# Kernel tuning notes

Hardware: AMD Instinct MI355X
Metric: run time of the kernel (lower is better)

Reference implementation:

```python
import jax, jax.numpy as jnp
import numpy as np

B = 8          # graphs per batch
N_PER = 8192   # nodes per graph (equal-sized graphs -> static topk shapes)
N = B * N_PER  # 65536 total nodes
DEG = 16
E = DEG * N    # 1,048,576 edges
C = 64         # conv_width


def setup_inputs() -> dict:
    key = jax.random.key(0)
    ks = jax.random.split(key, 32)
    epg = E // B
    g = jnp.arange(E, dtype=jnp.int32) // epg            # graph id per edge
    src = jax.random.randint(ks[0], (E,), 0, N_PER, dtype=jnp.int32) + g * N_PER
    dst = jax.random.randint(ks[1], (E,), 0, N_PER, dtype=jnp.int32) + g * N_PER

    def w(k, shape, fan_in):
        return (jax.random.normal(k, shape) / np.sqrt(fan_in)).astype(jnp.float32)

    inp = {
        "x": jax.random.normal(ks[2], (N, 2), dtype=jnp.float32),
        "edge_index": jnp.stack([src, dst]),
        # SAGEConv i: out = mean_agg @ wl + x @ wr + b
        "w1l": w(ks[3], (2, C), 2),  "w1r": w(ks[4], (2, C), 2),  "b1": jnp.zeros((C,), jnp.float32),
        "w2l": w(ks[5], (C, C), C),  "w2r": w(ks[6], (C, C), C),  "b2": jnp.zeros((C,), jnp.float32),
        "w3l": w(ks[7], (C, C), C),  "w3r": w(ks[8], (C, C), C),  "b3": jnp.zeros((C,), jnp.float32),
        # GCNConv
        "w4": w(ks[9], (C, C), C),   "b4": jnp.zeros((C,), jnp.float32),
        # TopKPooling score vectors
        "p1": w(ks[10], (C,), C), "p2": w(ks[11], (C,), C),
        "p3": w(ks[12], (C,), C), "p4": w(ks[13], (C,), C),
        # MLP head
        "lw1": w(ks[14], (2 * C, 128), 2 * C), "lb1": jnp.zeros((128,), jnp.float32),
        "lw2": w(ks[15], (128, 64), 128),      "lb2": jnp.zeros((64,), jnp.float32),
        "lw3": w(ks[16], (64, 1), 64),         "lb3": jnp.zeros((1,), jnp.float32),
    }
    return inp


def _sage(x, src, dst, em, wl, wr, b):
    # PyG SAGEConv: lin_l(mean of in-neighbors) + lin_r(x); masked edges contribute 0
    n = x.shape[0]
    s = jax.ops.segment_sum(x[src] * em[:, None], dst, num_segments=n)
    cnt = jax.ops.segment_sum(em, dst, num_segments=n)
    mean = s / jnp.maximum(cnt, 1.0)[:, None]
    return mean @ wl + x @ wr + b


def _gcn(x, src, dst, em, w, b):
    # PyG GCNConv with added self-loops, symmetric normalization
    n = x.shape[0]
    xw = x @ w
    deg = jax.ops.segment_sum(em, dst, num_segments=n) + 1.0  # +1 self-loop
    dinv = jax.lax.rsqrt(deg)
    coef = (dinv[src] * dinv[dst] * em)[:, None]
    agg = jax.ops.segment_sum(xw[src] * coef, dst, num_segments=n)
    return agg + xw / deg[:, None] + b  # self-loop term: deg^-0.5 * deg^-0.5


def _pool(x, src, dst, em, p, nb):
    # TopKPooling(ratio=0.5): score = x.p/||p||, keep top half per graph, scale by tanh
    n = x.shape[0]
    npg = n // nb
    k = npg // 2
    score = x @ p / jnp.linalg.norm(p)
    _, idx = jax.lax.top_k(score.reshape(nb, npg), k)          # [nb, k] local idx
    perm = (idx + (jnp.arange(nb, dtype=idx.dtype) * npg)[:, None]).reshape(-1)
    xn = x[perm] * jnp.tanh(score[perm])[:, None]
    o2n = jnp.full((n,), -1, jnp.int32).at[perm].set(jnp.arange(nb * k, dtype=jnp.int32))
    ns, nd = o2n[src], o2n[dst]
    nm = em * ((ns >= 0) & (nd >= 0)).astype(em.dtype)         # filter_adj via mask
    return xn, jnp.maximum(ns, 0), jnp.maximum(nd, 0), nm


def _readout(x, nb):
    # cat([global_max_pool, global_mean_pool])
    npg = x.shape[0] // nb
    batch = jnp.repeat(jnp.arange(nb), npg)
    mx = jax.ops.segment_max(x, batch, num_segments=nb)
    mn = jax.ops.segment_sum(x, batch, num_segments=nb) / npg
    return jnp.concatenate([mx, mn], axis=1)


def reference(x, edge_index, w1l, w1r, b1, w2l, w2r, b2, w3l, w3r, b3, w4, b4,
              p1, p2, p3, p4, lw1, lb1, lw2, lb2, lw3, lb3):
    src, dst = edge_index[0], edge_index[1]
    em = jnp.ones((src.shape[0],), jnp.float32)

    h = jax.nn.relu(_sage(x, src, dst, em, w1l, w1r, b1))
    h, src, dst, em = _pool(h, src, dst, em, p1, B)
    x1 = _readout(h, B)

    h = jax.nn.relu(_sage(h, src, dst, em, w2l, w2r, b2))
    h, src, dst, em = _pool(h, src, dst, em, p2, B)
    x2 = _readout(h, B)

    h = jax.nn.relu(_sage(h, src, dst, em, w3l, w3r, b3))
    h, src, dst, em = _pool(h, src, dst, em, p3, B)
    x3 = _readout(h, B)  # computed but unused, matching original (x = x1 + x2)

    h = jax.nn.relu(_gcn(h, src, dst, em, w4, b4))
    h, src, dst, em = _pool(h, src, dst, em, p4, B)
    x4 = _readout(h, B)  # computed but unused, matching original

    z = x1 + x2
    z = jax.nn.relu(z @ lw1 + lb1)
    z = jax.nn.relu(z @ lw2 + lb2)
    return z @ lw3 + lb3  # [B, 1]
```

## Files before the change

kernel.cpp:

```cpp
#include <hip/hip_runtime.h>
#include <stdint.h>
#include <math.h>

#define NB 8
#define NPG0 8192
#define EPG 131072
#define P1 16
#define MAXDEG 64

__global__ __launch_bounds__(1024)
void k_aggp(const int* __restrict__ src, const int* __restrict__ dst,
            const float* __restrict__ x, float* __restrict__ partial)
{
    __shared__ float acc[3 * 2048];
    int b = blockIdx.x;
    int g = b >> 6, qq = (b >> 4) & 3, sl = b & 15;
    int tid = threadIdx.x;
    float4* acc4 = (float4*)acc;
    float4 z4 = make_float4(0.f, 0.f, 0.f, 0.f);
    acc4[tid] = z4;
    if (tid < 512) acc4[1024 + tid] = z4;
    __syncthreads();
    int e0 = g * EPG + sl * (EPG / P1);
    int nbase = g * NPG0 + qq * 2048;
    const float2* x2 = reinterpret_cast<const float2*>(x);
    #pragma unroll
    for (int k = 0; k < 2; ++k) {
        int e = e0 + (k * 1024 + tid) * 4;
        int4 d4 = *reinterpret_cast<const int4*>(dst + e);
        unsigned l0 = (unsigned)(d4.x - nbase), l1 = (unsigned)(d4.y - nbase);
        unsigned l2 = (unsigned)(d4.z - nbase), l3 = (unsigned)(d4.w - nbase);
        bool v0 = l0 < 2048u, v1 = l1 < 2048u, v2 = l2 < 2048u, v3 = l3 < 2048u;
        if (v0 | v1 | v2 | v3) {
            int4 s4 = *reinterpret_cast<const int4*>(src + e);
            if (v0) { float2 xv = x2[s4.x]; atomicAdd(&acc[l0], xv.x);
                      atomicAdd(&acc[2048 + l0], xv.y); atomicAdd(&acc[4096 + l0], 1.0f); }
            if (v1) { float2 xv = x2[s4.y]; atomicAdd(&acc[l1], xv.x);
                      atomicAdd(&acc[2048 + l1], xv.y); atomicAdd(&acc[4096 + l1], 1.0f); }
            if (v2) { float2 xv = x2[s4.z]; atomicAdd(&acc[l2], xv.x);
                      atomicAdd(&acc[2048 + l2], xv.y); atomicAdd(&acc[4096 + l2], 1.0f); }
            if (v3) { float2 xv = x2[s4.w]; atomicAdd(&acc[l3], xv.x);
                      atomicAdd(&acc[2048 + l3], xv.y); atomicAdd(&acc[4096 + l3], 1.0f); }
        }
    }
    __syncthreads();
    float4* o = (float4*)(partial + (size_t)b * 6144);
    o[tid] = acc4[tid];
    if (tid < 512) o[1024 + tid] = acc4[1024 + tid];
}

__global__ __launch_bounds__(256)
void k_sage1f(const float* __restrict__ partial, const float* __restrict__ x,
              const float* __restrict__ w1l, const float* __restrict__ w1r,
              const float* __restrict__ b1, const float* __restrict__ p1,
              float2* __restrict__ mv, float* __restrict__ s1)
{
    int tid = threadIdx.x;
    int node = blockIdx.x * 256 + tid;
    int g = node >> 13, local = node & (NPG0 - 1);
    int qq = local >> 11, ll = local & 2047;
    const float* p = partial + (size_t)(g * 64 + qq * 16) * 6144 + ll;
    float s0 = 0.f, s1v = 0.f, sc = 0.f;
    #pragma unroll
    for (int q = 0; q < 16; ++q) {
        const float* pq = p + (size_t)q * 6144;
        s0 += pq[0]; s1v += pq[2048]; sc += pq[4096];
    }
    float inv = 1.0f / fmaxf(sc, 1.0f);
    float m0 = s0 * inv, m1 = s1v * inv;
    float2 xv = reinterpret_cast<const float2*>(x)[node];
    mv[node] = make_float2(m0, m1);
    float num = 0.f, nrm = 0.f;
    #pragma unroll 8
    for (int c = 0; c < 64; ++c) {
        float h = fmaxf(m0 * w1l[c] + m1 * w1l[64 + c]
                      + xv.x * w1r[c] + xv.y * w1r[64 + c] + b1[c], 0.0f);
        float pv = p1[c];
        num += h * pv; nrm += pv * pv;
    }
    s1[node] = num / sqrtf(nrm);
}

__device__ __forceinline__ unsigned scan1024(unsigned val, volatile unsigned* ws)
{
    int tid = threadIdx.x, lane = tid & 63, wid = tid >> 6;
    unsigned sc = val;
    #pragma unroll
    for (int off = 1; off < 64; off <<= 1) {
        unsigned t = __shfl_up(sc, off);
        if (lane >= off) sc += t;
    }
    if (lane == 63) ws[wid] = sc;
    __syncthreads();
    if (tid < 16) {
        unsigned w = ws[tid];
        #pragma unroll
        for (int off = 1; off < 16; off <<= 1) {
            unsigned t = __shfl_up(w, off);
            if (tid >= off) w += t;
        }
        ws[tid] = w;
    }
    __syncthreads();
    return sc + (wid ? ws[wid - 1] : 0u);
}

__global__ __launch_bounds__(1024)
void k_pool1(const float* __restrict__ score, int* __restrict__ n2o,
             int* __restrict__ o2n, int K, int* __restrict__ zbuf)
{
    const int NPG = 8192;
    __shared__ unsigned key[NPG];
    __shared__ unsigned hist[1024];
    __shared__ unsigned ws[16];
    __shared__ unsigned long long cand[1024];
    __shared__ int sT1, sR1, sT2, sR2, selCnt, c3;
    int g = blockIdx.x, tid = threadIdx.x;
    for (int i = tid; i < 4096; i += 1024) zbuf[g * 4096 + i] = 0;
    if (tid == 0) { selCnt = 0; c3 = 0; }
    hist[tid] = 0u;
    for (int i = tid; i < NPG; i += 1024) o2n[g * NPG + i] = -1;
    __syncthreads();
    for (int i = tid; i < NPG; i += 1024) {
        unsigned b = __float_as_uint(score[g * NPG + i]);
        unsigned u = (b & 0x80000000u) ? ~b : (b | 0x80000000u);
        key[i] = u;
        atomicAdd(&hist[u >> 22], 1u);
    }
    __syncthreads();
    {
        unsigned S = scan1024(hist[1023 - tid], ws);
        int b = 1023 - tid;
        unsigned h = hist[b];
        if (S >= (unsigned)K && S - h < (unsigned)K) { sT1 = b; sR1 = K - (int)(S - h); }
    }
    __syncthreads();
    int T1 = sT1, R1 = sR1;
    for (int i = tid; i < NPG; i += 1024) {
        if ((int)(key[i] >> 22) > T1) {
            int s = atomicAdd(&selCnt, 1);
            int oldid = g * NPG + i;
            n2o[g * K + s] = oldid;
            o2n[oldid] = g * K + s;
        }
    }
    __syncthreads();
    hist[tid] = 0u;
    __syncthreads();
    for (int i = tid; i < NPG; i += 1024)
        if ((int)(key[i] >> 22) == T1) atomicAdd(&hist[(key[i] >> 12) & 1023u], 1u);
    __syncthreads();
    {
        unsigned S = scan1024(hist[1023 - tid], ws);
        int b = 1023 - tid;
        unsigned h = hist[b];
        if (S >= (unsigned)R1 && S - h < (unsigned)R1) { sT2 = b; sR2 = R1 - (int)(S - h); }
    }
    __syncthreads();
    int T2 = sT2, R2 = sR2;
    for (int i = tid; i < NPG; i += 1024) {
        unsigned u = key[i];
        if ((int)(u >> 22) == T1) {
            int b2 = (int)((u >> 12) & 1023u);
            if (b2 > T2) {
                int s = atomicAdd(&selCnt, 1);
                int oldid = g * NPG + i;
                n2o[g * K + s] = oldid;
                o2n[oldid] = g * K + s;
            } else if (b2 == T2) {
                int c = atomicAdd(&c3, 1);
                if (c < 1024)
                    cand[c] = ((unsigned long long)u << 32) | (unsigned)(NPG - 1 - i);
            }
        }
    }
    __syncthreads();
    int M = min(c3, 1024);
    for (int t = tid; t < M; t += 1024) {
        unsigned long long k0 = cand[t];
        int rank = 0;
        for (int j = 0; j < M; ++j) rank += (cand[j] > k0);
        if (rank < R2) {
            int i = NPG - 1 - (int)(k0 & 0xFFFFFFFFu);
            int s = atomicAdd(&selCnt, 1);
            int oldid = g * NPG + i;
            n2o[g * K + s] = oldid;
            o2n[oldid] = g * K + s;
        }
    }
}

__global__ __launch_bounds__(1024)
void k_pool2(const float* __restrict__ score, int* __restrict__ n2o, int K)
{
    const int NPG = 4096;
    __shared__ unsigned key[NPG];
    __shared__ unsigned hist[1024];
    __shared__ unsigned ws[16];
    __shared__ unsigned long long cand[1024];
    __shared__ int sT1, sR1, sT2, sR2, selCnt, c3;
    int g = blockIdx.x, tid = threadIdx.x;
    if (tid == 0) { selCnt = 0; c3 = 0; }
    hist[tid] = 0u;
    __syncthreads();
    for (int i = tid; i < NPG; i += 1024) {
        unsigned b = __float_as_uint(score[g * NPG + i]);
        unsigned u = (b & 0x80000000u) ? ~b : (b | 0x80000000u);
        key[i] = u;
        atomicAdd(&hist[u >> 22], 1u);
    }
    __syncthreads();
    {
        unsigned S = scan1024(hist[1023 - tid], ws);
        int b = 1023 - tid;
        unsigned h = hist[b];
        if (S >= (unsigned)K && S - h < (unsigned)K) { sT1 = b; sR1 = K - (int)(S - h); }
    }
    __syncthreads();
    int T1 = sT1, R1 = sR1;
    for (int i = tid; i < NPG; i += 1024) {
        if ((int)(key[i] >> 22) > T1)
            n2o[g * K + atomicAdd(&selCnt, 1)] = g * NPG + i;
    }
    __syncthreads();
    hist[tid] = 0u;
    __syncthreads();
    for (int i = tid; i < NPG; i += 1024)
        if ((int)(key[i] >> 22) == T1) atomicAdd(&hist[(key[i] >> 12) & 1023u], 1u);
    __syncthreads();
    {
        unsigned S = scan1024(hist[1023 - tid], ws);
        int b = 1023 - tid;
        unsigned h = hist[b];
        if (S >= (unsigned)R1 && S - h < (unsigned)R1) { sT2 = b; sR2 = R1 - (int)(S - h); }
    }
    __syncthreads();
    int T2 = sT2, R2 = sR2;
    for (int i = tid; i < NPG; i += 1024) {
        unsigned u = key[i];
        if ((int)(u >> 22) == T1) {
            int b2 = (int)((u >> 12) & 1023u);
            if (b2 > T2) {
                n2o[g * K + atomicAdd(&selCnt, 1)] = g * NPG + i;
            } else if (b2 == T2) {
                int c = atomicAdd(&c3, 1);
                if (c < 1024)
                    cand[c] = ((unsigned long long)u << 32) | (unsigned)(NPG - 1 - i);
            }
        }
    }
    __syncthreads();
    int M = min(c3, 1024);
    for (int t = tid; t < M; t += 1024) {
        unsigned long long k0 = cand[t];
        int rank = 0;
        for (int j = 0; j < M; ++j) rank += (cand[j] > k0);
        if (rank < R2) {
            int i = NPG - 1 - (int)(k0 & 0xFFFFFFFFu);
            n2o[g * K + atomicAdd(&selCnt, 1)] = g * NPG + i;
        }
    }
}

__global__ __launch_bounds__(1024)
void k_mid(const float2* __restrict__ mv, const float* __restrict__ x,
           const float* __restrict__ s1, const int* __restrict__ n2o,
           const float* __restrict__ w1l, const float* __restrict__ w1r,
           const float* __restrict__ b1, int npg, float* __restrict__ hp,
           float* __restrict__ pmx, float* __restrict__ psm,
           const int* __restrict__ src, const int* __restrict__ dst,
           const int* __restrict__ o2n, int* __restrict__ cnt,
           int* __restrict__ slots)
{
    __shared__ float4 smx[1024], ssm[1024];
    int b = blockIdx.x;
    int tid = threadIdx.x;
    if (b >= 128) {
        int e = ((b - 128) * 1024 + tid) * 4;
        int4 s4 = *reinterpret_cast<const int4*>(src + e);
        int4 d4 = *reinterpret_cast<const int4*>(dst + e);
        #pragma unroll
        for (int i = 0; i < 4; ++i) {
            int sv = (i == 0) ? s4.x : (i == 1) ? s4.y : (i == 2) ? s4.z : s4.w;
            int dv = (i == 0) ? d4.x : (i == 1) ? d4.y : (i == 2) ? d4.z : d4.w;
            int ns = o2n[sv], nd = o2n[dv];
            if (ns >= 0 && nd >= 0) {
                int pos = atomicAdd(&cnt[nd], 1);
                if (pos < MAXDEG) slots[nd * MAXDEG + pos] = ns;
            }
        }
        return;
    }
    int g = b >> 4, sl = b & 15;
    int cg = tid & 15, rsl = tid >> 4;
    int rpb = npg >> 4;
    int c0 = cg * 4;
    float4 wl0 = *reinterpret_cast<const float4*>(w1l + c0);
    float4 wl1 = *reinterpret_cast<const float4*>(w1l + 64 + c0);
    float4 wr0 = *reinterpret_cast<const float4*>(w1r + c0);
    float4 wr1 = *reinterpret_cast<const float4*>(w1r + 64 + c0);
    float4 bb  = *reinterpret_cast<const float4*>(b1 + c0);
    const float2* x2 = reinterpret_cast<const float2*>(x);
    float4 mx = make_float4(-INFINITY, -INFINITY, -INFINITY, -INFINITY);
    float4 sm = make_float4(0.f, 0.f, 0.f, 0.f);
    for (int r = rsl; r < rpb; r += 64) {
        int row = g * npg + sl * rpb + r;
        int old = n2o[row];
        float2 m = mv[old];
        float2 xv = x2[old];
        float t = tanhf(s1[old]);
        float4 v;
        v.x = fmaxf(m.x * wl0.x + m.y * wl1.x + xv.x * wr0.x + xv.y * wr1.x + bb.x, 0.f) * t;
        v.y = fmaxf(m.x * wl0.y + m.y * wl1.y + xv.x * wr0.y + xv.y * wr1.y + bb.y, 0.f) * t;
        v.z = fmaxf(m.x * wl0.z + m.y * wl1.z + xv.x * wr0.z + xv.y * wr1.z + bb.z, 0.f) * t;
        v.w = fmaxf(m.x * wl0.w + m.y * wl1.w + xv.x * wr0.w + xv.y * wr1.w + bb.w, 0.f) * t;
        reinterpret_cast<float4*>(hp)[row * 16 + cg] = v;
        mx.x = fmaxf(mx.x, v.x); mx.y = fmaxf(mx.y, v.y);
        mx.z = fmaxf(mx.z, v.z); mx.w = fmaxf(mx.w, v.w);
        sm.x += v.x; sm.y += v.y; sm.z += v.z; sm.w += v.w;
    }
    smx[tid] = mx; ssm[tid] = sm;
    __syncthreads();
    for (int s = 32; s >= 1; s >>= 1) {
        if (rsl < s) {
            float4 a = smx[tid], bq = smx[tid + s * 16];
            a.x = fmaxf(a.x, bq.x); a.y = fmaxf(a.y, bq.y);
            a.z = fmaxf(a.z, bq.z); a.w = fmaxf(a.w, bq.w);
            smx[tid] = a;
            float4 c = ssm[tid], d = ssm[tid + s * 16];
            c.x += d.x; c.y += d.y; c.z += d.z; c.w += d.w;
            ssm[tid] = c;
        }
        __syncthreads();
    }
    if (rsl == 0) {
        reinterpret_cast<float4*>(pmx)[(g * 16 + sl) * 16 + cg] = smx[tid];
        reinterpret_cast<float4*>(psm)[(g * 16 + sl) * 16 + cg] = ssm[tid];
    }
}

__global__ __launch_bounds__(256)
void k_sage2(const float* __restrict__ hp, const int* __restrict__ cnt,
             const int* __restrict__ slots,
             const float* __restrict__ w2l, const float* __restrict__ w2r,
             const float* __restrict__ b2, const float* __restrict__ p2,
             float* __restrict__ h2, float* __restrict__ s2)
{
    __shared__ float Xs[64 * 128];
    __shared__ float Wt[64 * 128];
    int tid = threadIdx.x, blk = blockIdx.x;

    #pragma unroll
    for (int i = 0; i < 32; ++i) {
        int idx = i * 256 + tid;
        int k = idx >> 6, c = idx & 63;
        float w = (k < 64) ? w2l[k * 64 + c] : w2r[(k - 64) * 64 + c];
        int slot = (k >> 2) ^ ((c >> 2) & 7);
        Wt[c * 128 + slot * 4 + (k & 3)] = w;
    }

    {
        int n = tid >> 2, p = tid & 3;
        int j = blk * 64 + n;
        int dg = cnt[j];
        int lim = min(dg, MAXDEG);
        const int* sl = slots + j * MAXDEG;
        const float4* hp4 = reinterpret_cast<const float4*>(hp);
        float4 a[4];
        #pragma unroll
        for (int u = 0; u < 4; ++u) a[u] = make_float4(0.f, 0.f, 0.f, 0.f);
        int e = 0;
        for (; e + 1 < lim; e += 2) {
            int r0 = sl[e] * 16 + p * 4;
            int r1 = sl[e + 1] * 16 + p * 4;
            float4 v[4], u4[4];
            #pragma unroll
            for (int u = 0; u < 4; ++u) v[u] = hp4[r0 + u];
            #pragma unroll
            for (int u = 0; u < 4; ++u) u4[u] = hp4[r1 + u];
            #pragma unroll
            for (int u = 0; u < 4; ++u) {
                a[u].x += v[u].x + u4[u].x; a[u].y += v[u].y + u4[u].y;
                a[u].z += v[u].z + u4[u].z; a[u].w += v[u].w + u4[u].w;
            }
        }
        if (e < lim) {
            int r0 = sl[e] * 16 + p * 4;
            #pragma unroll
            for (int u = 0; u < 4; ++u) {
                float4 v = hp4[r0 + u];
                a[u].x += v.x; a[u].y += v.y; a[u].z += v.z; a[u].w += v.w;
            }
        }
        float inv = 1.0f / fmaxf((float)dg, 1.0f);
        int swz = (n >> 2) & 7;
        float4* X4 = reinterpret_cast<float4*>(Xs);
        #pragma unroll
        for (int u = 0; u < 4; ++u) {
            float4 m = a[u];
            m.x *= inv; m.y *= inv; m.z *= inv; m.w *= inv;
            X4[n * 32 + ((p * 4 + u) ^ swz)] = m;
        }
        #pragma unroll
        for (int u = 0; u < 4; ++u)
            X4[n * 32 + ((16 + p * 4 + u) ^ swz)] = hp4[j * 16 + p * 4 + u];
    }
    __syncthreads();

    int rt = tid >> 4, ct = tid & 15;
    int r0 = rt * 4, c0 = ct * 4;
    int swa = rt & 7, swb = ct & 7;
    const float4* Xf = reinterpret_cast<const float4*>(Xs);
    const float4* Wf = reinterpret_cast<const float4*>(Wt);
    float acc[4][4];
    #pragma unroll
    for (int i = 0; i < 4; ++i)
        #pragma unroll
        for (int jq = 0; jq < 4; ++jq) acc[i][jq] = 0.f;
    #pragma unroll 8
    for (int ks = 0; ks < 32; ++ks) {
        float4 aa[4], bb[4];
        #pragma unroll
        for (int i = 0; i < 4; ++i) aa[i] = Xf[(r0 + i) * 32 + (ks ^ swa)];
        #pragma unroll
        for (int jq = 0; jq < 4; ++jq) bb[jq] = Wf[(c0 + jq) * 32 + (ks ^ swb)];
        #pragma unroll
        for (int i = 0; i < 4; ++i)
            #pragma unroll
            for (int jq = 0; jq < 4; ++jq)
                acc[i][jq] += aa[i].x * bb[jq].x + aa[i].y * bb[jq].y
                            + aa[i].z * bb[jq].z + aa[i].w * bb[jq].w;
    }

    float4 b2v = reinterpret_cast<const float4*>(b2)[ct];
    float4 p2v = reinterpret_cast<const float4*>(p2)[ct];
    float nrm = p2v.x * p2v.x + p2v.y * p2v.y + p2v.z * p2v.z + p2v.w * p2v.w;
    float sp[4];
    float4* h2f = reinterpret_cast<float4*>(h2);
    #pragma unroll
    for (int i = 0; i < 4; ++i) {
        float4 o;
        o.x = fmaxf(acc[i][0] + b2v.x, 0.f);
        o.y = fmaxf(acc[i][1] + b2v.y, 0.f);
        o.z = fmaxf(acc[i][2] + b2v.z, 0.f);
        o.w = fmaxf(acc[i][3] + b2v.w, 0.f);
        h2f[(blk * 64 + r0 + i) * 16 + ct] = o;
        sp[i] = o.x * p2v.x + o.y * p2v.y + o.z * p2v.z + o.w * p2v.w;
    }
    #pragma unroll
    for (int o = 1; o < 16; o <<= 1) {
        #pragma unroll
        for (int i = 0; i < 4; ++i) sp[i] += __shfl_xor(sp[i], o);
        nrm += __shfl_xor(nrm, o);
    }
    if (ct == 0) {
        float r = rsqrtf(nrm);
        #pragma unroll
        for (int i = 0; i < 4; ++i) s2[blk * 64 + r0 + i] = sp[i] * r;
    }
}

__global__ __launch_bounds__(1024)
void k_readout_p(const float* __restrict__ h, const int* __restrict__ n2o,
                 const float* __restrict__ sc, int npg,
                 float* __restrict__ pmx, float* __restrict__ psm)
{
    int g = blockIdx.x >> 4, sl = blockIdx.x & 15;
    int tid = threadIdx.x;
    int cg = tid & 15, rsl = tid >> 4;
    int rpb = npg >> 4;
    float4 mx = make_float4(-INFINITY, -INFINITY, -INFINITY, -INFINITY);
    float4 sm = make_float4(0.f, 0.f, 0.f, 0.f);
    for (int r = rsl; r < rpb; r += 64) {
        int row = g * npg + sl * rpb + r;
        int oldid = n2o[row];
        float t = tanhf(sc[oldid]);
        float4 v = reinterpret_cast<const float4*>(h)[oldid * 16 + cg];
        v.x *= t; v.y *= t; v.z *= t; v.w *= t;
        mx.x = fmaxf(mx.x, v.x); mx.y = fmaxf(mx.y, v.y);
        mx.z = fmaxf(mx.z, v.z); mx.w = fmaxf(mx.w, v.w);
        sm.x += v.x; sm.y += v.y; sm.z += v.z; sm.w += v.w;
    }
    __shared__ float4 smx[1024], ssm[1024];
    smx[tid] = mx; ssm[tid] = sm;
    __syncthreads();
    for (int s = 32; s >= 1; s >>= 1) {
        if (rsl < s) {
            float4 a = smx[tid], b = smx[tid + s * 16];
            a.x = fmaxf(a.x, b.x); a.y = fmaxf(a.y, b.y);
            a.z = fmaxf(a.z, b.z); a.w = fmaxf(a.w, b.w);
            smx[tid] = a;
            float4 c = ssm[tid], d = ssm[tid + s * 16];
            c.x += d.x; c.y += d.y; c.z += d.z; c.w += d.w;
            ssm[tid] = c;
        }
        __syncthreads();
    }
    if (rsl == 0) {
        reinterpret_cast<float4*>(pmx)[(g * 16 + sl) * 16 + cg] = smx[tid];
        reinterpret_cast<float4*>(psm)[(g * 16 + sl) * 16 + cg] = ssm[tid];
    }
}

__global__ __launch_bounds__(128)
void k_mlp(const float* __restrict__ pmx1, const float* __restrict__ psm1,
           const float* __restrict__ pmx2, const float* __restrict__ psm2,
           int npg1, int npg2,
           const float* __restrict__ lw1, const float* __restrict__ lb1,
           const float* __restrict__ lw2, const float* __restrict__ lb2,
           const float* __restrict__ lw3, const float* __restrict__ lb3,
           float* __restrict__ out)
{
    __shared__ float z[NB][128], o1[NB][128], o2[NB][64];
    int tid = threadIdx.x;
    for (int g = 0; g < NB; ++g) {
        float v;
        if (tid < 64) {
            float m1 = -INFINITY, m2 = -INFINITY;
            #pragma unroll
            for (int sl = 0; sl < 16; ++sl) {
                m1 = fmaxf(m1, pmx1[(g * 16 + sl) * 64 + tid]);
                m2 = fmaxf(m2, pmx2[(g * 16 + sl) * 64 + tid]);
            }
            v = m1 + m2;
        } else {
            int ch = tid - 64;
            float s1 = 0.f, s2 = 0.f;
            #pragma unroll
            for (int sl = 0; sl < 16; ++sl) {
                s1 += psm1[(g * 16 + sl) * 64 + ch];
                s2 += psm2[(g * 16 + sl) * 64 + ch];
            }
            v = s1 / (float)npg1 + s2 / (float)npg2;
        }
        z[g][tid] = v;
    }
    __syncthreads();
    for (int g = 0; g < NB; ++g) {
        float a = lb1[tid];
        for (int i = 0; i < 128; ++i) a += z[g][i] * lw1[i * 128 + tid];
        o1[g][tid] = fmaxf(a, 0.0f);
    }
    __syncthreads();
    if (tid < 64) {
        for (int g = 0; g < NB; ++g) {
            float a = lb2[tid];
            for (int i = 0; i < 128; ++i) a += o1[g][i] * lw2[i * 64 + tid];
            o2[g][tid] = fmaxf(a, 0.0f);
        }
    }
    __syncthreads();
    if (tid < NB) {
        int g = tid;
        float a = lb3[0];
        for (int i = 0; i < 64; ++i) a += o2[g][i] * lw3[i];
        out[g] = a;
    }
}

extern "C" void kernel_launch(void* const* d_in, const int* in_sizes, int n_in,
                              void* d_out, int out_size, void* d_ws, size_t ws_size,
                              hipStream_t stream)
{
    (void)n_in; (void)out_size; (void)ws_size;
    const float* x   = (const float*)d_in[0];
    const int*   ei  = (const int*)d_in[1];
    const float* w1l = (const float*)d_in[2];
    const float* w1r = (const float*)d_in[3];
    const float* b1  = (const float*)d_in[4];
    const float* w2l = (const float*)d_in[5];
    const float* w2r = (const float*)d_in[6];
    const float* b2  = (const float*)d_in[7];
    const float* p1  = (const float*)d_in[13];
    const float* p2  = (const float*)d_in[14];
    const float* lw1 = (const float*)d_in[17];
    const float* lb1 = (const float*)d_in[18];
    const float* lw2 = (const float*)d_in[19];
    const float* lb2 = (const float*)d_in[20];
    const float* lw3 = (const float*)d_in[21];
    const float* lb3 = (const float*)d_in[22];

    const int N0   = in_sizes[0] / 2;
    const int E    = in_sizes[1] / 2;
    const int K1   = NPG0 / 2;
    const int N1   = NB * K1;
    const int K2   = K1 / 2;

    const int* src = ei;
    const int* dst = ei + E;

    char* w = (char*)d_ws;
    auto alloc = [&](size_t bytes) -> char* {
        char* p = w;
        w += (bytes + 255) & ~(size_t)255;
        return p;
    };
    float*  partial = (float*)alloc((size_t)NB * 4 * P1 * 6144 * 4);
    float2* mv    = (float2*)alloc((size_t)N0 * 8);
    int*    cnt2  = (int*)alloc((size_t)N1 * 4);
    int*    slots = (int*)alloc((size_t)N1 * MAXDEG * 4);
    float*  s1    = (float*)alloc((size_t)N0 * 4);
    int*    o2n1  = (int*)alloc((size_t)N0 * 4);
    int*    n2o1  = (int*)alloc((size_t)N1 * 4);
    float*  h1p   = (float*)alloc((size_t)N1 * 64 * 4);
    float*  h2    = (float*)alloc((size_t)N1 * 64 * 4);
    float*  s2    = (float*)alloc((size_t)N1 * 4);
    int*    n2o2  = (int*)alloc((size_t)(NB * K2) * 4);
    float*  pmx1  = (float*)alloc((size_t)NB * 16 * 64 * 4);
    float*  psm1  = (float*)alloc((size_t)NB * 16 * 64 * 4);
    float*  pmx2  = (float*)alloc((size_t)NB * 16 * 64 * 4);
    float*  psm2  = (float*)alloc((size_t)NB * 16 * 64 * 4);

    k_aggp<<<NB * 4 * P1, 1024, 0, stream>>>(src, dst, x, partial);
    k_sage1f<<<N0 / 256, 256, 0, stream>>>(partial, x, w1l, w1r, b1, p1, mv, s1);
    k_pool1<<<NB, 1024, 0, stream>>>(s1, n2o1, o2n1, K1, cnt2);
    k_mid<<<128 + 256, 1024, 0, stream>>>(mv, x, s1, n2o1, w1l, w1r, b1, K1,
                                          h1p, pmx1, psm1,
                                          src, dst, o2n1, cnt2, slots);
    k_sage2<<<N1 / 64, 256, 0, stream>>>(h1p, cnt2, slots, w2l, w2r, b2, p2, h2, s2);
    k_pool2<<<NB, 1024, 0, stream>>>(s2, n2o2, K2);
    k_readout_p<<<NB * 16, 1024, 0, stream>>>(h2, n2o2, s2, K2, pmx2, psm2);
    k_mlp<<<1, 128, 0, stream>>>(pmx1, psm1, pmx2, psm2, K1, K2,
                                 lw1, lb1, lw2, lb2, lw3, lb3, (float*)d_out);
}
```

Baseline: 121.9 us.

## Fuse pool2, readout and MLP into one kernel with flag-based sync

The last three launches (top-k pool of layer 2, partial readout, MLP head) become a single kernel. The first 8 blocks do per-graph selection and publish a release flag. Readout blocks spin on their graph's flag, and the last block to finish, found through an atomic counter, runs the MLP. This removes two kernel launch gaps at the tail. It relies on the producer blocks being scheduled before or alongside the spinning consumers, which risks deadlock if they are not resident together.

```diff
diff --git a/kernel.cpp b/kernel.cpp
--- a/kernel.cpp
+++ b/kernel.cpp
@@ -107,7 +107,8 @@
 
 __global__ __launch_bounds__(1024)
 void k_pool1(const float* __restrict__ score, int* __restrict__ n2o,
-             int* __restrict__ o2n, int K, int* __restrict__ zbuf)
+             int* __restrict__ o2n, int K, int* __restrict__ zbuf,
+             int* __restrict__ flags, int* __restrict__ counter)
 {
     const int NPG = 8192;
     __shared__ unsigned key[NPG];
@@ -117,6 +118,8 @@
     __shared__ int sT1, sR1, sT2, sR2, selCnt, c3;
     int g = blockIdx.x, tid = threadIdx.x;
     for (int i = tid; i < 4096; i += 1024) zbuf[g * 4096 + i] = 0;
+    if (g == 0 && tid < 8) flags[tid] = 0;
+    if (g == 0 && tid == 8) *counter = 0;
     if (tid == 0) { selCnt = 0; c3 = 0; }
     hist[tid] = 0u;
     for (int i = tid; i < NPG; i += 1024) o2n[g * NPG + i] = -1;
@@ -186,78 +189,6 @@
             int oldid = g * NPG + i;
             n2o[g * K + s] = oldid;
             o2n[oldid] = g * K + s;
-        }
-    }
-}
-
-__global__ __launch_bounds__(1024)
-void k_pool2(const float* __restrict__ score, int* __restrict__ n2o, int K)
-{
-    const int NPG = 4096;
-    __shared__ unsigned key[NPG];
-    __shared__ unsigned hist[1024];
-    __shared__ unsigned ws[16];
-    __shared__ unsigned long long cand[1024];
-    __shared__ int sT1, sR1, sT2, sR2, selCnt, c3;
-    int g = blockIdx.x, tid = threadIdx.x;
-    if (tid == 0) { selCnt = 0; c3 = 0; }
-    hist[tid] = 0u;
-    __syncthreads();
-    for (int i = tid; i < NPG; i += 1024) {
-        unsigned b = __float_as_uint(score[g * NPG + i]);
-        unsigned u = (b & 0x80000000u) ? ~b : (b | 0x80000000u);
-        key[i] = u;
-        atomicAdd(&hist[u >> 22], 1u);
-    }
-    __syncthreads();
-    {
-        unsigned S = scan1024(hist[1023 - tid], ws);
-        int b = 1023 - tid;
-        unsigned h = hist[b];
-        if (S >= (unsigned)K && S - h < (unsigned)K) { sT1 = b; sR1 = K - (int)(S - h); }
-    }
-    __syncthreads();
-    int T1 = sT1, R1 = sR1;
-    for (int i = tid; i < NPG; i += 1024) {
-        if ((int)(key[i] >> 22) > T1)
-            n2o[g * K + atomicAdd(&selCnt, 1)] = g * NPG + i;
-    }
-    __syncthreads();
-    hist[tid] = 0u;
-    __syncthreads();
-    for (int i = tid; i < NPG; i += 1024)
-        if ((int)(key[i] >> 22) == T1) atomicAdd(&hist[(key[i] >> 12) & 1023u], 1u);
-    __syncthreads();
-    {
-        unsigned S = scan1024(hist[1023 - tid], ws);
-        int b = 1023 - tid;
-        unsigned h = hist[b];
-        if (S >= (unsigned)R1 && S - h < (unsigned)R1) { sT2 = b; sR2 = R1 - (int)(S - h); }
-    }
-    __syncthreads();
-    int T2 = sT2, R2 = sR2;
-    for (int i = tid; i < NPG; i += 1024) {
-        unsigned u = key[i];
-        if ((int)(u >> 22) == T1) {
-            int b2 = (int)((u >> 12) & 1023u);
-            if (b2 > T2) {
-                n2o[g * K + atomicAdd(&selCnt, 1)] = g * NPG + i;
-            } else if (b2 == T2) {
-                int c = atomicAdd(&c3, 1);
-                if (c < 1024)
-                    cand[c] = ((unsigned long long)u << 32) | (unsigned)(NPG - 1 - i);
-            }
-        }
-    }
-    __syncthreads();
-    int M = min(c3, 1024);
-    for (int t = tid; t < M; t += 1024) {
-        unsigned long long k0 = cand[t];
-        int rank = 0;
-        for (int j = 0; j < M; ++j) rank += (cand[j] > k0);
-        if (rank < R2) {
-            int i = NPG - 1 - (int)(k0 & 0xFFFFFFFFu);
-            n2o[g * K + atomicAdd(&selCnt, 1)] = g * NPG + i;
         }
     }
 }
@@ -461,34 +392,121 @@
 }
 
 __global__ __launch_bounds__(1024)
-void k_readout_p(const float* __restrict__ h, const int* __restrict__ n2o,
-                 const float* __restrict__ sc, int npg,
-                 float* __restrict__ pmx, float* __restrict__ psm)
-{
-    int g = blockIdx.x >> 4, sl = blockIdx.x & 15;
-    int tid = threadIdx.x;
+void k_tail(const float* __restrict__ s2, const float* __restrict__ h2,
+            int* __restrict__ n2o2, int* __restrict__ flags, int* __restrict__ counter,
+            const float* __restrict__ pmx1, const float* __restrict__ psm1,
+            float* __restrict__ pmx2, float* __restrict__ psm2,
+            const float* __restrict__ lw1, const float* __restrict__ lb1,
+            const float* __restrict__ lw2, const float* __restrict__ lb2,
+            const float* __restrict__ lw3, const float* __restrict__ lb3,
+            float* __restrict__ out)
+{
+    const int NPG = 4096, K = 2048;
+    __shared__ __align__(16) char smem[33 * 1024];
+    __shared__ unsigned wsS[16];
+    __shared__ int sT1, sR1, sT2, sR2, selCnt, c3, isLast;
+    int b = blockIdx.x, tid = threadIdx.x;
+
+    if (b < 8) {
+        unsigned* key  = (unsigned*)smem;
+        unsigned* hist = (unsigned*)(smem + 16 * 1024);
+        unsigned long long* cand = (unsigned long long*)(smem + 20 * 1024);
+        int g = b;
+        if (tid == 0) { selCnt = 0; c3 = 0; }
+        hist[tid] = 0u;
+        __syncthreads();
+        for (int i = tid; i < NPG; i += 1024) {
+            unsigned kb = __float_as_uint(s2[g * NPG + i]);
+            unsigned u = (kb & 0x80000000u) ? ~kb : (kb | 0x80000000u);
+            key[i] = u;
+            atomicAdd(&hist[u >> 22], 1u);
+        }
+        __syncthreads();
+        {
+            unsigned S = scan1024(hist[1023 - tid], wsS);
+            int bb = 1023 - tid;
+            unsigned h = hist[bb];
+            if (S >= (unsigned)K && S - h < (unsigned)K) { sT1 = bb; sR1 = K - (int)(S - h); }
+        }
+        __syncthreads();
+        int T1 = sT1, R1 = sR1;
+        for (int i = tid; i < NPG; i += 1024) {
+            if ((int)(key[i] >> 22) > T1)
+                n2o2[g * K + atomicAdd(&selCnt, 1)] = g * NPG + i;
+        }
+        __syncthreads();
+        hist[tid] = 0u;
+        __syncthreads();
+        for (int i = tid; i < NPG; i += 1024)
+            if ((int)(key[i] >> 22) == T1) atomicAdd(&hist[(key[i] >> 12) & 1023u], 1u);
+        __syncthreads();
+        {
+            unsigned S = scan1024(hist[1023 - tid], wsS);
+            int bb = 1023 - tid;
+            unsigned h = hist[bb];
+            if (S >= (unsigned)R1 && S - h < (unsigned)R1) { sT2 = bb; sR2 = R1 - (int)(S - h); }
+        }
+        __syncthreads();
+        int T2 = sT2, R2 = sR2;
+        for (int i = tid; i < NPG; i += 1024) {
+            unsigned u = key[i];
+            if ((int)(u >> 22) == T1) {
+                int b2 = (int)((u >> 12) & 1023u);
+                if (b2 > T2) {
+                    n2o2[g * K + atomicAdd(&selCnt, 1)] = g * NPG + i;
+                } else if (b2 == T2) {
+                    int c = atomicAdd(&c3, 1);
+                    if (c < 1024)
+                        cand[c] = ((unsigned long long)u << 32) | (unsigned)(NPG - 1 - i);
+                }
+            }
+        }
+        __syncthreads();
+        int M = min(c3, 1024);
+        for (int t = tid; t < M; t += 1024) {
+            unsigned long long k0 = cand[t];
+            int rank = 0;
+            for (int j = 0; j < M; ++j) rank += (cand[j] > k0);
+            if (rank < R2)
+                n2o2[g * K + atomicAdd(&selCnt, 1)] = g * NPG + (NPG - 1 - (int)(k0 & 0xFFFFFFFFu));
+        }
+        __threadfence();
+        __syncthreads();
+        if (tid == 0)
+            __hip_atomic_store(&flags[g], 1, __ATOMIC_RELEASE, __HIP_MEMORY_SCOPE_AGENT);
+        return;
+    }
+
+    int rb = b - 8;
+    int g = rb >> 4, sl = rb & 15;
+    if (tid == 0) {
+        while (__hip_atomic_load(&flags[g], __ATOMIC_ACQUIRE, __HIP_MEMORY_SCOPE_AGENT) == 0)
+            __builtin_amdgcn_s_sleep(8);
+    }
+    __syncthreads();
+    float4* smx = (float4*)smem;
+    float4* ssm = (float4*)(smem + 16 * 1024);
     int cg = tid & 15, rsl = tid >> 4;
-    int rpb = npg >> 4;
+    int rpb = K >> 4;
     float4 mx = make_float4(-INFINITY, -INFINITY, -INFINITY, -INFINITY);
     float4 sm = make_float4(0.f, 0.f, 0.f, 0.f);
     for (int r = rsl; r < rpb; r += 64) {
-        int row = g * npg + sl * rpb + r;
-        int oldid = n2o[row];
-        float t = tanhf(sc[oldid]);
-        float4 v = reinterpret_cast<const float4*>(h)[oldid * 16 + cg];
+        int row = g * K + sl * rpb + r;
+        int oldid = n2o2[row];
+        float t = tanhf(s2[oldid]);
+        float4 v = reinterpret_cast<const float4*>(h2)[oldid * 16 + cg];
         v.x *= t; v.y *= t; v.z *= t; v.w *= t;
         mx.x = fmaxf(mx.x, v.x); mx.y = fmaxf(mx.y, v.y);
         mx.z = fmaxf(mx.z, v.z); mx.w = fmaxf(mx.w, v.w);
         sm.x += v.x; sm.y += v.y; sm.z += v.z; sm.w += v.w;
     }
-    __shared__ float4 smx[1024], ssm[1024];
     smx[tid] = mx; ssm[tid] = sm;
     __syncthreads();
     for (int s = 32; s >= 1; s >>= 1) {
         if (rsl < s) {
-            float4 a = smx[tid], b = smx[tid + s * 16];
-            a.x = fmaxf(a.x, b.x); a.y = fmaxf(a.y, b.y);
-            a.z = fmaxf(a.z, b.z); a.w = fmaxf(a.w, b.w);
+            float4 a = smx[tid], bq = smx[tid + s * 16];
+            a.x = fmaxf(a.x, bq.x); a.y = fmaxf(a.y, bq.y);
+            a.z = fmaxf(a.z, bq.z); a.w = fmaxf(a.w, bq.w);
             smx[tid] = a;
             float4 c = ssm[tid], d = ssm[tid + s * 16];
             c.x += d.x; c.y += d.y; c.z += d.z; c.w += d.w;
@@ -497,64 +515,67 @@
         __syncthreads();
     }
     if (rsl == 0) {
-        reinterpret_cast<float4*>(pmx)[(g * 16 + sl) * 16 + cg] = smx[tid];
-        reinterpret_cast<float4*>(psm)[(g * 16 + sl) * 16 + cg] = ssm[tid];
-    }
-}
-
-__global__ __launch_bounds__(128)
-void k_mlp(const float* __restrict__ pmx1, const float* __restrict__ psm1,
-           const float* __restrict__ pmx2, const float* __restrict__ psm2,
-           int npg1, int npg2,
-           const float* __restrict__ lw1, const float* __restrict__ lb1,
-           const float* __restrict__ lw2, const float* __restrict__ lb2,
-           const float* __restrict__ lw3, const float* __restrict__ lb3,
-           float* __restrict__ out)
-{
-    __shared__ float z[NB][128], o1[NB][128], o2[NB][64];
-    int tid = threadIdx.x;
-    for (int g = 0; g < NB; ++g) {
-        float v;
-        if (tid < 64) {
-            float m1 = -INFINITY, m2 = -INFINITY;
-            #pragma unroll
-            for (int sl = 0; sl < 16; ++sl) {
-                m1 = fmaxf(m1, pmx1[(g * 16 + sl) * 64 + tid]);
-                m2 = fmaxf(m2, pmx2[(g * 16 + sl) * 64 + tid]);
+        reinterpret_cast<float4*>(pmx2)[(g * 16 + sl) * 16 + cg] = smx[tid];
+        reinterpret_cast<float4*>(psm2)[(g * 16 + sl) * 16 + cg] = ssm[tid];
+    }
+    __threadfence();
+    __syncthreads();
+    if (tid == 0) {
+        int old = __hip_atomic_fetch_add(counter, 1, __ATOMIC_ACQ_REL, __HIP_MEMORY_SCOPE_AGENT);
+        isLast = (old == 127);
+    }
+    __syncthreads();
+    if (!isLast) return;
+
+    float* z  = (float*)smem;
+    float* o1 = (float*)(smem + 4 * 1024);
+    float* o2 = (float*)(smem + 8 * 1024);
+    if (tid < 128) {
+        for (int gg = 0; gg < NB; ++gg) {
+            float v;
+            if (tid < 64) {
+                float m1 = -INFINITY, m2 = -INFINITY;
+                #pragma unroll
+                for (int s = 0; s < 16; ++s) {
+                    m1 = fmaxf(m1, pmx1[(gg * 16 + s) * 64 + tid]);
+                    m2 = fmaxf(m2, pmx2[(gg * 16 + s) * 64 + tid]);
+                }
+                v = m1 + m2;
+            } else {
+                int ch = tid - 64;
+                float a1 = 0.f, a2 = 0.f;
+                #pragma unroll
+                for (int s = 0; s < 16; ++s) {
+                    a1 += psm1[(gg * 16 + s) * 64 + ch];
+                    a2 += psm2[(gg * 16 + s) * 64 + ch];
+                }
+                v = a1 / 4096.0f + a2 / 2048.0f;
             }
-            v = m1 + m2;
-        } else {
-            int ch = tid - 64;
-            float s1 = 0.f, s2 = 0.f;
-            #pragma unroll
-            for (int sl = 0; sl < 16; ++sl) {
-                s1 += psm1[(g * 16 + sl) * 64 + ch];
-                s2 += psm2[(g * 16 + sl) * 64 + ch];
-            }
-            v = s1 / (float)npg1 + s2 / (float)npg2;
-        }
-        z[g][tid] = v;
-    }
-    __syncthreads();
-    for (int g = 0; g < NB; ++g) {
-        float a = lb1[tid];
-        for (int i = 0; i < 128; ++i) a += z[g][i] * lw1[i * 128 + tid];
-        o1[g][tid] = fmaxf(a, 0.0f);
+            z[gg * 128 + tid] = v;
+        }
+    }
+    __syncthreads();
+    if (tid < 128) {
+        for (int gg = 0; gg < NB; ++gg) {
+            float a = lb1[tid];
+            for (int i = 0; i < 128; ++i) a += z[gg * 128 + i] * lw1[i * 128 + tid];
+            o1[gg * 128 + tid] = fmaxf(a, 0.0f);
+        }
     }
     __syncthreads();
     if (tid < 64) {
-        for (int g = 0; g < NB; ++g) {
+        for (int gg = 0; gg < NB; ++gg) {
             float a = lb2[tid];
-            for (int i = 0; i < 128; ++i) a += o1[g][i] * lw2[i * 64 + tid];
-            o2[g][tid] = fmaxf(a, 0.0f);
+            for (int i = 0; i < 128; ++i) a += o1[gg * 128 + i] * lw2[i * 64 + tid];
+            o2[gg * 64 + tid] = fmaxf(a, 0.0f);
         }
     }
     __syncthreads();
     if (tid < NB) {
-        int g = tid;
+        int gg = tid;
         float a = lb3[0];
-        for (int i = 0; i < 64; ++i) a += o2[g][i] * lw3[i];
-        out[g] = a;
+        for (int i = 0; i < 64; ++i) a += o2[gg * 64 + i] * lw3[i];
+        out[gg] = a;
     }
 }
 
@@ -610,16 +631,17 @@
     float*  psm1  = (float*)alloc((size_t)NB * 16 * 64 * 4);
     float*  pmx2  = (float*)alloc((size_t)NB * 16 * 64 * 4);
     float*  psm2  = (float*)alloc((size_t)NB * 16 * 64 * 4);
+    int*    flags = (int*)alloc(64);
+    int*    counter = (int*)alloc(64);
 
     k_aggp<<<NB * 4 * P1, 1024, 0, stream>>>(src, dst, x, partial);
     k_sage1f<<<N0 / 256, 256, 0, stream>>>(partial, x, w1l, w1r, b1, p1, mv, s1);
-    k_pool1<<<NB, 1024, 0, stream>>>(s1, n2o1, o2n1, K1, cnt2);
+    k_pool1<<<NB, 1024, 0, stream>>>(s1, n2o1, o2n1, K1, cnt2, flags, counter);
     k_mid<<<128 + 256, 1024, 0, stream>>>(mv, x, s1, n2o1, w1l, w1r, b1, K1,
                                           h1p, pmx1, psm1,
                                           src, dst, o2n1, cnt2, slots);
     k_sage2<<<N1 / 64, 256, 0, stream>>>(h1p, cnt2, slots, w2l, w2r, b2, p2, h2, s2);
-    k_pool2<<<NB, 1024, 0, stream>>>(s2, n2o2, K2);
-    k_readout_p<<<NB * 16, 1024, 0, stream>>>(h2, n2o2, s2, K2, pmx2, psm2);
-    k_mlp<<<1, 128, 0, stream>>>(pmx1, psm1, pmx2, psm2, K1, K2,
-                                 lw1, lb1, lw2, lb2, lw3, lb3, (float*)d_out);
-}
+    k_tail<<<8 + 128, 1024, 0, stream>>>(s2, h2, n2o2, flags, counter,
+                                         pmx1, psm1, pmx2, psm2,
+                                         lw1, lb1, lw2, lb2, lw3, lb3, (float*)d_out);
+}
```

Measured after the change: 171.5 us. 40.7% more time.

## Recompute pooled layer-1 features on the fly in sage2 instead of materializing them

Applied to the files above, without the earlier changes.

Stops writing the 64-channel pooled hidden features of layer 1 to memory. Instead, each node's 2-dim mean, 2-dim input and tanh score are packed into a compact float4 plus scalar, and sage2 recomputes the 64-wide features per gathered neighbor from these, with edge slots now holding original node ids. This trades a large gather of 256-byte rows for 20-byte gathers plus extra FMAs per edge. The MLP head is also restructured to load each weight once and reuse it across all graphs.

```diff
diff --git a/kernel.cpp b/kernel.cpp
--- a/kernel.cpp
+++ b/kernel.cpp
@@ -53,7 +53,8 @@
 void k_sage1f(const float* __restrict__ partial, const float* __restrict__ x,
               const float* __restrict__ w1l, const float* __restrict__ w1r,
               const float* __restrict__ b1, const float* __restrict__ p1,
-              float2* __restrict__ mv, float* __restrict__ s1)
+              float4* __restrict__ mvx, float* __restrict__ th,
+              float* __restrict__ s1)
 {
     int tid = threadIdx.x;
     int node = blockIdx.x * 256 + tid;
@@ -69,7 +70,7 @@
     float inv = 1.0f / fmaxf(sc, 1.0f);
     float m0 = s0 * inv, m1 = s1v * inv;
     float2 xv = reinterpret_cast<const float2*>(x)[node];
-    mv[node] = make_float2(m0, m1);
+    mvx[node] = make_float4(m0, m1, xv.x, xv.y);
     float num = 0.f, nrm = 0.f;
     #pragma unroll 8
     for (int c = 0; c < 64; ++c) {
@@ -78,7 +79,9 @@
         float pv = p1[c];
         num += h * pv; nrm += pv * pv;
     }
-    s1[node] = num / sqrtf(nrm);
+    float score = num / sqrtf(nrm);
+    s1[node] = score;
+    th[node] = tanhf(score);
 }
 
 __device__ __forceinline__ unsigned scan1024(unsigned val, volatile unsigned* ws)
@@ -263,10 +266,10 @@
 }
 
 __global__ __launch_bounds__(1024)
-void k_mid(const float2* __restrict__ mv, const float* __restrict__ x,
-           const float* __restrict__ s1, const int* __restrict__ n2o,
+void k_mid(const float4* __restrict__ mvx, const float* __restrict__ th,
+           const int* __restrict__ n2o,
            const float* __restrict__ w1l, const float* __restrict__ w1r,
-           const float* __restrict__ b1, int npg, float* __restrict__ hp,
+           const float* __restrict__ b1, int npg,
            float* __restrict__ pmx, float* __restrict__ psm,
            const int* __restrict__ src, const int* __restrict__ dst,
            const int* __restrict__ o2n, int* __restrict__ cnt,
@@ -286,7 +289,7 @@
             int ns = o2n[sv], nd = o2n[dv];
             if (ns >= 0 && nd >= 0) {
                 int pos = atomicAdd(&cnt[nd], 1);
-                if (pos < MAXDEG) slots[nd * MAXDEG + pos] = ns;
+                if (pos < MAXDEG) slots[nd * MAXDEG + pos] = sv;
             }
         }
         return;
@@ -300,21 +303,18 @@
     float4 wr0 = *reinterpret_cast<const float4*>(w1r + c0);
     float4 wr1 = *reinterpret_cast<const float4*>(w1r + 64 + c0);
     float4 bb  = *reinterpret_cast<const float4*>(b1 + c0);
-    const float2* x2 = reinterpret_cast<const float2*>(x);
     float4 mx = make_float4(-INFINITY, -INFINITY, -INFINITY, -INFINITY);
     float4 sm = make_float4(0.f, 0.f, 0.f, 0.f);
     for (int r = rsl; r < rpb; r += 64) {
         int row = g * npg + sl * rpb + r;
         int old = n2o[row];
-        float2 m = mv[old];
-        float2 xv = x2[old];
-        float t = tanhf(s1[old]);
+        float4 m = mvx[old];
+        float t = th[old];
         float4 v;
-        v.x = fmaxf(m.x * wl0.x + m.y * wl1.x + xv.x * wr0.x + xv.y * wr1.x + bb.x, 0.f) * t;
-        v.y = fmaxf(m.x * wl0.y + m.y * wl1.y + xv.x * wr0.y + xv.y * wr1.y + bb.y, 0.f) * t;
-        v.z = fmaxf(m.x * wl0.z + m.y * wl1.z + xv.x * wr0.z + xv.y * wr1.z + bb.z, 0.f) * t;
-        v.w = fmaxf(m.x * wl0.w + m.y * wl1.w + xv.x * wr0.w + xv.y * wr1.w + bb.w, 0.f) * t;
-        reinterpret_cast<float4*>(hp)[row * 16 + cg] = v;
+        v.x = fmaxf(m.x * wl0.x + m.y * wl1.x + m.z * wr0.x + m.w * wr1.x + bb.x, 0.f) * t;
+        v.y = fmaxf(m.x * wl0.y + m.y * wl1.y + m.z * wr0.y + m.w * wr1.y + bb.y, 0.f) * t;
+        v.z = fmaxf(m.x * wl0.z + m.y * wl1.z + m.z * wr0.z + m.w * wr1.z + bb.z, 0.f) * t;
+        v.w = fmaxf(m.x * wl0.w + m.y * wl1.w + m.z * wr0.w + m.w * wr1.w + bb.w, 0.f) * t;
         mx.x = fmaxf(mx.x, v.x); mx.y = fmaxf(mx.y, v.y);
         mx.z = fmaxf(mx.z, v.z); mx.w = fmaxf(mx.w, v.w);
         sm.x += v.x; sm.y += v.y; sm.z += v.z; sm.w += v.w;
@@ -340,8 +340,11 @@
 }
 
 __global__ __launch_bounds__(256)
-void k_sage2(const float* __restrict__ hp, const int* __restrict__ cnt,
+void k_sage2(const float4* __restrict__ mvx, const float* __restrict__ th,
+             const int* __restrict__ n2o, const int* __restrict__ cnt,
              const int* __restrict__ slots,
+             const float* __restrict__ w1l, const float* __restrict__ w1r,
+             const float* __restrict__ b1,
              const float* __restrict__ w2l, const float* __restrict__ w2r,
              const float* __restrict__ b2, const float* __restrict__ p2,
              float* __restrict__ h2, float* __restrict__ s2)
@@ -365,31 +368,46 @@
         int dg = cnt[j];
         int lim = min(dg, MAXDEG);
         const int* sl = slots + j * MAXDEG;
-        const float4* hp4 = reinterpret_cast<const float4*>(hp);
+        float4 wl0[4], wl1[4], wr0[4], wr1[4], bb[4];
+        #pragma unroll
+        for (int u = 0; u < 4; ++u) {
+            int c = p * 16 + u * 4;
+            wl0[u] = *reinterpret_cast<const float4*>(w1l + c);
+            wl1[u] = *reinterpret_cast<const float4*>(w1l + 64 + c);
+            wr0[u] = *reinterpret_cast<const float4*>(w1r + c);
+            wr1[u] = *reinterpret_cast<const float4*>(w1r + 64 + c);
+            bb[u]  = *reinterpret_cast<const float4*>(b1 + c);
+        }
+        auto hfun = [&](const float4& m, float t, int u) -> float4 {
+            float4 r;
+            r.x = fmaxf(m.x * wl0[u].x + m.y * wl1[u].x + m.z * wr0[u].x + m.w * wr1[u].x + bb[u].x, 0.f) * t;
+            r.y = fmaxf(m.x * wl0[u].y + m.y * wl1[u].y + m.z * wr0[u].y + m.w * wr1[u].y + bb[u].y, 0.f) * t;
+            r.z = fmaxf(m.x * wl0[u].z + m.y * wl1[u].z + m.z * wr0[u].z + m.w * wr1[u].z + bb[u].z, 0.f) * t;
+            r.w = fmaxf(m.x * wl0[u].w + m.y * wl1[u].w + m.z * wr0[u].w + m.w * wr1[u].w + bb[u].w, 0.f) * t;
+            return r;
+        };
         float4 a[4];
         #pragma unroll
         for (int u = 0; u < 4; ++u) a[u] = make_float4(0.f, 0.f, 0.f, 0.f);
         int e = 0;
         for (; e + 1 < lim; e += 2) {
-            int r0 = sl[e] * 16 + p * 4;
-            int r1 = sl[e + 1] * 16 + p * 4;
-            float4 v[4], u4[4];
-            #pragma unroll
-            for (int u = 0; u < 4; ++u) v[u] = hp4[r0 + u];
-            #pragma unroll
-            for (int u = 0; u < 4; ++u) u4[u] = hp4[r1 + u];
+            int o0 = sl[e], o1 = sl[e + 1];
+            float4 mA = mvx[o0]; float tA = th[o0];
+            float4 mB = mvx[o1]; float tB = th[o1];
             #pragma unroll
             for (int u = 0; u < 4; ++u) {
-                a[u].x += v[u].x + u4[u].x; a[u].y += v[u].y + u4[u].y;
-                a[u].z += v[u].z + u4[u].z; a[u].w += v[u].w + u4[u].w;
+                float4 vA = hfun(mA, tA, u), vB = hfun(mB, tB, u);
+                a[u].x += vA.x + vB.x; a[u].y += vA.y + vB.y;
+                a[u].z += vA.z + vB.z; a[u].w += vA.w + vB.w;
             }
         }
         if (e < lim) {
-            int r0 = sl[e] * 16 + p * 4;
+            int o0 = sl[e];
+            float4 mA = mvx[o0]; float tA = th[o0];
             #pragma unroll
             for (int u = 0; u < 4; ++u) {
-                float4 v = hp4[r0 + u];
-                a[u].x += v.x; a[u].y += v.y; a[u].z += v.z; a[u].w += v.w;
+                float4 vA = hfun(mA, tA, u);
+                a[u].x += vA.x; a[u].y += vA.y; a[u].z += vA.z; a[u].w += vA.w;
             }
         }
         float inv = 1.0f / fmaxf((float)dg, 1.0f);
@@ -401,9 +419,11 @@
             m.x *= inv; m.y *= inv; m.z *= inv; m.w *= inv;
             X4[n * 32 + ((p * 4 + u) ^ swz)] = m;
         }
+        int os = n2o[j];
+        float4 mS = mvx[os]; float tS = th[os];
         #pragma unroll
         for (int u = 0; u < 4; ++u)
-            X4[n * 32 + ((16 + p * 4 + u) ^ swz)] = hp4[j * 16 + p * 4 + u];
+            X4[n * 32 + ((16 + p * 4 + u) ^ swz)] = hfun(mS, tS, u);
     }
     __syncthreads();
 
@@ -536,18 +556,30 @@
         z[g][tid] = v;
     }
     __syncthreads();
-    for (int g = 0; g < NB; ++g) {
-        float a = lb1[tid];
-        for (int i = 0; i < 128; ++i) a += z[g][i] * lw1[i * 128 + tid];
-        o1[g][tid] = fmaxf(a, 0.0f);
+    {
+        float a[NB];
+        #pragma unroll
+        for (int g = 0; g < NB; ++g) a[g] = lb1[tid];
+        for (int i = 0; i < 128; ++i) {
+            float wv = lw1[i * 128 + tid];
+            #pragma unroll
+            for (int g = 0; g < NB; ++g) a[g] += z[g][i] * wv;
+        }
+        #pragma unroll
+        for (int g = 0; g < NB; ++g) o1[g][tid] = fmaxf(a[g], 0.0f);
     }
     __syncthreads();
     if (tid < 64) {
-        for (int g = 0; g < NB; ++g) {
-            float a = lb2[tid];
-            for (int i = 0; i < 128; ++i) a += o1[g][i] * lw2[i * 64 + tid];
-            o2[g][tid] = fmaxf(a, 0.0f);
-        }
+        float a[NB];
+        #pragma unroll
+        for (int g = 0; g < NB; ++g) a[g] = lb2[tid];
+        for (int i = 0; i < 128; ++i) {
+            float wv = lw2[i * 64 + tid];
+            #pragma unroll
+            for (int g = 0; g < NB; ++g) a[g] += o1[g][i] * wv;
+        }
+        #pragma unroll
+        for (int g = 0; g < NB; ++g) o2[g][tid] = fmaxf(a[g], 0.0f);
     }
     __syncthreads();
     if (tid < NB) {
@@ -596,13 +628,13 @@
         return p;
     };
     float*  partial = (float*)alloc((size_t)NB * 4 * P1 * 6144 * 4);
-    float2* mv    = (float2*)alloc((size_t)N0 * 8);
+    float4* mvx   = (float4*)alloc((size_t)N0 * 16);
+    float*  th    = (float*)alloc((size_t)N0 * 4);
     int*    cnt2  = (int*)alloc((size_t)N1 * 4);
     int*    slots = (int*)alloc((size_t)N1 * MAXDEG * 4);
     float*  s1    = (float*)alloc((size_t)N0 * 4);
     int*    o2n1  = (int*)alloc((size_t)N0 * 4);
     int*    n2o1  = (int*)alloc((size_t)N1 * 4);
-    float*  h1p   = (float*)alloc((size_t)N1 * 64 * 4);
     float*  h2    = (float*)alloc((size_t)N1 * 64 * 4);
     float*  s2    = (float*)alloc((size_t)N1 * 4);
     int*    n2o2  = (int*)alloc((size_t)(NB * K2) * 4);
@@ -612,12 +644,13 @@
     float*  psm2  = (float*)alloc((size_t)NB * 16 * 64 * 4);
 
     k_aggp<<<NB * 4 * P1, 1024, 0, stream>>>(src, dst, x, partial);
-    k_sage1f<<<N0 / 256, 256, 0, stream>>>(partial, x, w1l, w1r, b1, p1, mv, s1);
+    k_sage1f<<<N0 / 256, 256, 0, stream>>>(partial, x, w1l, w1r, b1, p1, mvx, th, s1);
     k_pool1<<<NB, 1024, 0, stream>>>(s1, n2o1, o2n1, K1, cnt2);
-    k_mid<<<128 + 256, 1024, 0, stream>>>(mv, x, s1, n2o1, w1l, w1r, b1, K1,
-                                          h1p, pmx1, psm1,
+    k_mid<<<128 + 256, 1024, 0, stream>>>(mvx, th, n2o1, w1l, w1r, b1, K1,
+                                          pmx1, psm1,
                                           src, dst, o2n1, cnt2, slots);
-    k_sage2<<<N1 / 64, 256, 0, stream>>>(h1p, cnt2, slots, w2l, w2r, b2, p2, h2, s2);
+    k_sage2<<<N1 / 64, 256, 0, stream>>>(mvx, th, n2o1, cnt2, slots,
+                                         w1l, w1r, b1, w2l, w2r, b2, p2, h2, s2);
     k_pool2<<<NB, 1024, 0, stream>>>(s2, n2o2, K2);
     k_readout_p<<<NB * 16, 1024, 0, stream>>>(h2, n2o2, s2, K2, pmx2, psm2);
     k_mlp<<<1, 128, 0, stream>>>(pmx1, psm1, pmx2, psm2, K1, K2,
```

New measurement: 121.0 us. About the same (-0.8%).
